# Kernel optimization log

Hardware: AMD Instinct MI355X
Metric: run time of the kernel (lower is better)

## Reference

```python
import jax, jax.numpy as jnp
import numpy as np

DECAY = 0.99
EPS = 1e-05


def setup_inputs() -> dict:
    key = jax.random.key(0)
    k1, k2 = jax.random.split(key)
    B, T, D, K = 16, 4096, 256, 1024
    z = jax.random.normal(k1, (B, T, D), dtype=jnp.float32)
    embedding = jax.random.normal(k2, (D, K), dtype=jnp.float32)
    cluster_size = jnp.zeros((K,), dtype=jnp.float32)
    embedding_mean = embedding.copy()  # torch init: embedding.clone()
    return {"z": z, "embedding": embedding, "cluster_size": cluster_size,
            "embedding_mean": embedding_mean}


def reference(z, embedding, cluster_size, embedding_mean):
    """Training-mode forward of CodebookEMA (proj=False).

    z:              [B, T, D]
    embedding:      [D, K] codebook buffer
    cluster_size:   [K]    EMA cluster counts
    embedding_mean: [D, K] EMA cluster sums
    Returns (z_q, commitment_loss, codebook_loss, code,
             new_embedding, new_cluster_size, new_embedding_mean).
    """
    B, T, D = z.shape
    K = embedding.shape[1]
    z_flat = z.reshape(B * T, D)

    # squared-distance quantization: ||z||^2 - 2 z.E + ||e||^2  -> [BT, K]
    dist = ((z_flat * z_flat).sum(1, keepdims=True)
            - 2.0 * (z_flat @ embedding)
            + (embedding * embedding).sum(0)[None, :])
    idx = jnp.argmin(dist, axis=1)              # [BT]
    code = idx.reshape(B, T)

    # EMA codebook update (no one-hot materialization; use segment sums)
    counts = jax.ops.segment_sum(jnp.ones_like(idx, dtype=z.dtype), idx,
                                 num_segments=K)               # [K]
    emb_sum = jax.ops.segment_sum(z_flat, idx, num_segments=K).T  # [D, K]
    new_cluster_size = cluster_size * DECAY + (1.0 - DECAY) * counts
    new_embedding_mean = embedding_mean * DECAY + (1.0 - DECAY) * emb_sum
    n = new_cluster_size.sum()
    cs_norm = (new_cluster_size + EPS) / (n + K * EPS) * n     # Laplace-smoothed
    new_embedding = new_embedding_mean / cs_norm[None, :]      # [D, K]

    # dequantize with the *updated* codebook (as in the torch control flow)
    z_q = new_embedding.T[code]                                # [B, T, D]

    commitment_loss = ((jax.lax.stop_gradient(z_q) - z) ** 2).mean(axis=(1, 2))
    codebook_loss = jnp.zeros((B,), dtype=z.dtype)
    z_q = z + jax.lax.stop_gradient(z_q - z)  # straight-through estimator
    return (z_q, commitment_loss, codebook_loss, code,
            new_embedding, new_cluster_size, new_embedding_mean)
```

## Files before the change

### kernel.cpp

```cpp
#include <hip/hip_runtime.h>
#include <cfloat>
#include <climits>
#include <cstdint>

#define B_ 16
#define T_ 4096
#define D_ 256
#define K_ 1024
#define BT_ 65536
#define DECAYF 0.99f
#define OMDECAYF 0.01f
#define EPSF 1e-5f
#define TAUGAP 0.125f
#define CHUNK 32
#define GROUP 16
#define RMARGIN 0.01f

typedef float f32x4 __attribute__((ext_vector_type(4)));
typedef _Float16 f16x8 __attribute__((ext_vector_type(8)));

__device__ __forceinline__ void gload16(const void* g, void* l) {
    __builtin_amdgcn_global_load_lds(
        (const __attribute__((address_space(1))) void*)g,
        (__attribute__((address_space(3))) void*)l, 16, 0, 0);
}

__global__ void k_prep(const float* __restrict__ z, const float* __restrict__ E,
                       _Float16* __restrict__ zf, _Float16* __restrict__ EfT,
                       float* __restrict__ enorm, double* __restrict__ enorm64,
                       int* __restrict__ counts, int* __restrict__ nflag,
                       float* __restrict__ out_closs, float* __restrict__ out_cbl,
                       float* __restrict__ emb_sum) {
    int b = blockIdx.x;
    if (b < 8192) {
        int base = (b * 256 + threadIdx.x) * 8;
        float4 v0 = *(const float4*)(z + base);
        float4 v1 = *(const float4*)(z + base + 4);
        f16x8 h;
        h[0] = (_Float16)v0.x; h[1] = (_Float16)v0.y;
        h[2] = (_Float16)v0.z; h[3] = (_Float16)v0.w;
        h[4] = (_Float16)v1.x; h[5] = (_Float16)v1.y;
        h[6] = (_Float16)v1.z; h[7] = (_Float16)v1.w;
        *(f16x8*)(zf + base) = h;
    } else {
        __shared__ double rd[256];
        int n = b - 8192, d = threadIdx.x;
        float v = E[(size_t)d * K_ + n];
        EfT[(size_t)n * 256 + d] = (_Float16)v;
        rd[d] = (double)v * (double)v;
        __syncthreads();
        for (int st = 128; st > 0; st >>= 1) {
            if (d < st) rd[d] += rd[d + st];
            __syncthreads();
        }
        if (d == 0) { enorm[n] = (float)rd[0]; enorm64[n] = rd[0]; }
        emb_sum[(size_t)n * 256 + d] = 0.f;
        if (n < 4) counts[n * 256 + d] = 0;
        if (n == 4) {
            if (d < 16) out_closs[d] = 0.f;
            else if (d < 32) out_cbl[d - 16] = 0.f;
            else if (d == 32) *nflag = 0;
        }
    }
}

__global__ __launch_bounds__(512, 2) void k_argmin_mfma(
    const _Float16* __restrict__ zf, const _Float16* __restrict__ EfT,
    const float* __restrict__ enorm, int* __restrict__ code,
    int* __restrict__ flags, int* __restrict__ nflag, int* __restrict__ counts) {
    __shared__ _Float16 Ab[2][128 * 32];
    __shared__ _Float16 Bb[2][256 * 32];
    __shared__ float mg_d1[512];
    __shared__ int   mg_i1[512];
    __shared__ float mg_d2[512];

    const int t = threadIdx.x;
    const int row0 = blockIdx.x * 128;
    const int l = t & 63, wid = t >> 6;
    const int wr = wid >> 2, wc = wid & 3;
    const int lr = l & 15, lk = l >> 4;

    const int arow = t >> 2,          ablk = (t & 3) ^ ((arow >> 1) & 3);
    const int brow0 = t >> 2,         bblk0 = (t & 3) ^ ((brow0 >> 1) & 3);
    const int brow1 = (t + 512) >> 2, bblk1 = ((t + 512) & 3) ^ ((brow1 >> 1) & 3);

#define STAGE(it_, buf_) do {                                                       \
        int nc_ = (it_) >> 3; int kb_ = ((it_) & 7) * 32;                            \
        gload16(zf + (size_t)(row0 + arow) * 256 + kb_ + ablk * 8,                   \
                &Ab[buf_][(t & ~63) * 8]);                                           \
        gload16(EfT + (size_t)(nc_ * 256 + brow0) * 256 + kb_ + bblk0 * 8,           \
                &Bb[buf_][(t & ~63) * 8]);                                           \
        gload16(EfT + (size_t)(nc_ * 256 + brow1) * 256 + kb_ + bblk1 * 8,           \
                &Bb[buf_][((t + 512) & ~63) * 8]);                                   \
    } while (0)

    STAGE(0, 0);

    float D1[4][4], D2[4][4];
    int   I1[4][4];
    #pragma unroll
    for (int m = 0; m < 4; ++m)
        #pragma unroll
        for (int r = 0; r < 4; ++r) {
            D1[m][r] = FLT_MAX; D2[m][r] = FLT_MAX; I1[m][r] = 0x7fffffff;
        }

    f32x4 acc[4][4];
    for (int it = 0; it < 32; ++it) {
        if ((it & 7) == 0) {
            #pragma unroll
            for (int m = 0; m < 4; ++m)
                #pragma unroll
                for (int n = 0; n < 4; ++n) acc[m][n] = (f32x4){0.f, 0.f, 0.f, 0.f};
        }
        __syncthreads();
        if (it + 1 < 32) STAGE(it + 1, (it + 1) & 1);
        const _Float16* Abuf = Ab[it & 1];
        const _Float16* Bbuf = Bb[it & 1];
        f16x8 a[4], b[4];
        #pragma unroll
        for (int m = 0; m < 4; ++m) {
            int row = wr * 64 + m * 16 + lr;
            a[m] = *(const f16x8*)&Abuf[row * 32 + ((lk ^ ((row >> 1) & 3)) * 8)];
        }
        #pragma unroll
        for (int n = 0; n < 4; ++n) {
            int nn = wc * 64 + n * 16 + lr;
            b[n] = *(const f16x8*)&Bbuf[nn * 32 + ((lk ^ ((nn >> 1) & 3)) * 8)];
        }
        #pragma unroll
        for (int m = 0; m < 4; ++m)
            #pragma unroll
            for (int n = 0; n < 4; ++n)
                acc[m][n] = __builtin_amdgcn_mfma_f32_16x16x32_f16(
                    a[m], b[n], acc[m][n], 0, 0, 0);

        if ((it & 7) == 7) {
            int nc = it >> 3;
            float en[4];
            #pragma unroll
            for (int n = 0; n < 4; ++n)
                en[n] = enorm[nc * 256 + wc * 64 + n * 16 + lr];
            #pragma unroll
            for (int m = 0; m < 4; ++m)
                #pragma unroll
                for (int r = 0; r < 4; ++r)
                    #pragma unroll
                    for (int n = 0; n < 4; ++n) {
                        float dist = en[n] - 2.0f * acc[m][n][r];
                        int cg = nc * 256 + wc * 64 + n * 16 + lr;
                        if (dist < D1[m][r]) {
                            D2[m][r] = D1[m][r]; D1[m][r] = dist; I1[m][r] = cg;
                        } else D2[m][r] = fminf(D2[m][r], dist);
                    }
        }
    }
#undef STAGE

    #pragma unroll
    for (int m = 0; m < 4; ++m)
        #pragma unroll
        for (int r = 0; r < 4; ++r) {
            float d1 = D1[m][r], d2 = D2[m][r];
            int i1 = I1[m][r];
            #pragma unroll
            for (int mask = 1; mask < 16; mask <<= 1) {
                float pd1 = __shfl_xor(d1, mask);
                int   pi1 = __shfl_xor(i1, mask);
                float pd2 = __shfl_xor(d2, mask);
                if (pd1 < d1 || (pd1 == d1 && pi1 < i1)) {
                    d2 = fminf(d1, pd2); d1 = pd1; i1 = pi1;
                } else d2 = fminf(d2, pd1);
            }
            if (lr == 0) {
                int row = wr * 64 + m * 16 + lk * 4 + r;
                mg_d1[row * 4 + wc] = d1;
                mg_i1[row * 4 + wc] = i1;
                mg_d2[row * 4 + wc] = d2;
            }
        }
    __syncthreads();
    if (t < 128) {
        float b1 = FLT_MAX, b2 = FLT_MAX;
        int bi = 0x7fffffff;
        #pragma unroll
        for (int c = 0; c < 4; ++c) {
            float pd1 = mg_d1[t * 4 + c];
            int   pi1 = mg_i1[t * 4 + c];
            float pd2 = mg_d2[t * 4 + c];
            if (pd1 < b1 || (pd1 == b1 && pi1 < bi)) {
                b2 = fminf(b1, pd2); b1 = pd1; bi = pi1;
            } else b2 = fminf(b2, pd1);
        }
        code[row0 + t] = bi;
        atomicAdd(&counts[bi], 1);
        if (b2 - b1 < TAUGAP) {
            int pos = atomicAdd(nflag, 1);
            flags[pos] = row0 + t;
        }
    }
}

__global__ __launch_bounds__(256) void k_fixup(
    const float* __restrict__ z, const float* __restrict__ E,
    const float* __restrict__ enorm, const double* __restrict__ enorm64,
    const int* __restrict__ nflag, const int* __restrict__ flags,
    int* __restrict__ code, int* __restrict__ counts) {
    __shared__ float  zrows[GROUP][256];
    __shared__ int    rowid[GROUP];
    __shared__ float  bw[GROUP][4];
    __shared__ float  bestAll[GROUP];
    __shared__ int    ccnt[GROUP];
    __shared__ int    cand[GROUP][16];
    __shared__ double cdist[GROUP][16];

    const int t = threadIdx.x, w = t >> 6, l = t & 63;
    const int n = *nflag;
    const int ngroups = (n + GROUP - 1) / GROUP;

    for (int g = blockIdx.x; g < ngroups; g += gridDim.x) {
        __syncthreads();
        if (t < GROUP) {
            int idx = g * GROUP + t;
            rowid[t] = (idx < n) ? flags[idx] : -1;
            ccnt[t] = 0;
        }
        __syncthreads();
        {
            int i = t >> 4, s = t & 15;
            int r = rowid[i];
            const float* src = z + (size_t)(r < 0 ? 0 : r) * D_ + s * 16;
            float4 a0 = *(const float4*)(src + 0);
            float4 a1 = *(const float4*)(src + 4);
            float4 a2 = *(const float4*)(src + 8);
            float4 a3 = *(const float4*)(src + 12);
            *(float4*)&zrows[i][s * 16 + 0]  = a0;
            *(float4*)&zrows[i][s * 16 + 4]  = a1;
            *(float4*)&zrows[i][s * 16 + 8]  = a2;
            *(float4*)&zrows[i][s * 16 + 12] = a3;
        }
        __syncthreads();

        float acc[GROUP][4];
        #pragma unroll
        for (int i = 0; i < GROUP; ++i) {
            acc[i][0] = 0.f; acc[i][1] = 0.f; acc[i][2] = 0.f; acc[i][3] = 0.f;
        }
        const float* Ecol = E + 4 * t;
        for (int d = 0; d < D_; ++d) {
            float4 ev = *(const float4*)(Ecol + (size_t)d * K_);
            #pragma unroll
            for (int i = 0; i < GROUP; ++i) {
                float zd = zrows[i][d];
                acc[i][0] = fmaf(zd, ev.x, acc[i][0]);
                acc[i][1] = fmaf(zd, ev.y, acc[i][1]);
                acc[i][2] = fmaf(zd, ev.z, acc[i][2]);
                acc[i][3] = fmaf(zd, ev.w, acc[i][3]);
            }
        }
        float en0 = enorm[4 * t], en1 = enorm[4 * t + 1];
        float en2 = enorm[4 * t + 2], en3 = enorm[4 * t + 3];
        #pragma unroll
        for (int i = 0; i < GROUP; ++i) {
            acc[i][0] = en0 - 2.f * acc[i][0];
            acc[i][1] = en1 - 2.f * acc[i][1];
            acc[i][2] = en2 - 2.f * acc[i][2];
            acc[i][3] = en3 - 2.f * acc[i][3];
        }
        #pragma unroll
        for (int i = 0; i < GROUP; ++i) {
            float b = fminf(fminf(acc[i][0], acc[i][1]), fminf(acc[i][2], acc[i][3]));
            #pragma unroll
            for (int m = 1; m < 64; m <<= 1) b = fminf(b, __shfl_xor(b, m));
            if (l == 0) bw[i][w] = b;
        }
        __syncthreads();
        if (t < GROUP)
            bestAll[t] = fminf(fminf(bw[t][0], bw[t][1]), fminf(bw[t][2], bw[t][3]));
        __syncthreads();
        #pragma unroll
        for (int i = 0; i < GROUP; ++i) {
            float thr = bestAll[i] + RMARGIN;
            #pragma unroll
            for (int j = 0; j < 4; ++j) {
                if (acc[i][j] <= thr) {
                    int slot = atomicAdd(&ccnt[i], 1);
                    if (slot < 16) cand[i][slot] = 4 * t + j;
                }
            }
        }
        __syncthreads();
        for (int p = w; p < GROUP * 16; p += 4) {
            int i = p >> 4, s = p & 15;
            int cn = ccnt[i];
            if (rowid[i] < 0 || cn < 2 || s >= (cn < 16 ? cn : 16)) continue;
            int c = cand[i][s];
            double dot = 0.0;
            #pragma unroll
            for (int q = 0; q < 4; ++q) {
                int d = l * 4 + q;
                dot = fma((double)zrows[i][d], (double)E[(size_t)d * K_ + c], dot);
            }
            #pragma unroll
            for (int m = 1; m < 64; m <<= 1) dot += __shfl_xor(dot, m);
            if (l == 0) cdist[i][s] = enorm64[c] - 2.0 * dot;
        }
        __syncthreads();
        if (t < GROUP) {
            int r = rowid[t];
            if (r >= 0) {
                int cn = ccnt[t]; if (cn > 16) cn = 16;
                int newc;
                if (cn <= 1) {
                    newc = cand[t][0];
                } else {
                    double bd = DBL_MAX; int bi = INT_MAX;
                    for (int s = 0; s < cn; ++s) {
                        double dv = cdist[t][s]; int ci = cand[t][s];
                        if (dv < bd || (dv == bd && ci < bi)) { bd = dv; bi = ci; }
                    }
                    newc = bi;
                }
                int oldc = code[r];
                if (newc != oldc) {
                    code[r] = newc;
                    atomicSub(&counts[oldc], 1);
                    atomicAdd(&counts[newc], 1);
                }
            }
        }
    }
}

__global__ void k_scan(const int* __restrict__ counts, const float* __restrict__ cs,
                       int* __restrict__ offsets, int* __restrict__ cursor,
                       float* __restrict__ out_newcs, float* __restrict__ csnorm,
                       int* __restrict__ work, int* __restrict__ nwork) {
    __shared__ int   s[K_];
    __shared__ int   c[K_];
    __shared__ float red[K_];
    int t = threadIdx.x;
    int v = counts[t];
    int nch = (v + CHUNK - 1) / CHUNK;
    s[t] = v;
    c[t] = nch;
    float ncs = cs[t] * DECAYF + OMDECAYF * (float)v;
    out_newcs[t] = ncs;
    red[t] = ncs;
    __syncthreads();
    for (int d = 1; d < K_; d <<= 1) {
        int x = (t >= d) ? s[t - d] : 0;
        int y = (t >= d) ? c[t - d] : 0;
        __syncthreads();
        s[t] += x; c[t] += y;
        __syncthreads();
    }
    offsets[t] = s[t] - v;
    cursor[t]  = s[t] - v;
    if (t == K_ - 1) { offsets[K_] = s[t]; *nwork = c[t]; }
    int wbase = c[t] - nch;
    for (int j = 0; j < nch; ++j) work[wbase + j] = (t << 16) | j;
    for (int st = 512; st > 0; st >>= 1) {
        if (t < st) red[t] += red[t + st];
        __syncthreads();
    }
    float nsum = red[0];
    csnorm[t] = (ncs + EPSF) / (nsum + (float)K_ * EPSF) * nsum;
}

__global__ void k_sortidx(const int* __restrict__ code, int* __restrict__ cursor,
                          int* __restrict__ sorted) {
    int r = blockIdx.x * 256 + threadIdx.x;
    int cc = code[r];
    int pos = atomicAdd(&cursor[cc], 1);
    sorted[pos] = r;
}

__global__ void k_segsum(const float* __restrict__ z, const int* __restrict__ sorted,
                         const int* __restrict__ offsets, const int* __restrict__ work,
                         const int* __restrict__ nwork, float* __restrict__ emb_sum) {
    int NW = *nwork;
    int d = threadIdx.x;
    for (int i = blockIdx.x; i < NW; i += gridDim.x) {
        int wk = work[i];
        int k = wk >> 16, j = wk & 0xffff;
        int beg = offsets[k] + j * CHUNK;
        int end = min(beg + CHUNK, offsets[k + 1]);
        float s = 0.f;
        int idx = beg;
        for (; idx + 4 <= end; idx += 4) {
            int r0 = sorted[idx], r1 = sorted[idx + 1];
            int r2 = sorted[idx + 2], r3 = sorted[idx + 3];
            float v0 = z[(size_t)r0 * D_ + d];
            float v1 = z[(size_t)r1 * D_ + d];
            float v2 = z[(size_t)r2 * D_ + d];
            float v3 = z[(size_t)r3 * D_ + d];
            s += (v0 + v1) + (v2 + v3);
        }
        for (; idx < end; ++idx) s += z[(size_t)sorted[idx] * D_ + d];
        atomicAdd(&emb_sum[(size_t)k * D_ + d], s);
    }
}

__global__ void k_emb(const float* __restrict__ EM, const float* __restrict__ emb_sum,
                      const float* __restrict__ csnorm,
                      float* __restrict__ out_newemb, float* __restrict__ out_newem,
                      float* __restrict__ newembT) {
    int tid = blockIdx.x * 256 + threadIdx.x;
    int k = tid >> 8, d = tid & 255;
    float em  = EM[(size_t)d * K_ + k];
    float nem = em * DECAYF + OMDECAYF * emb_sum[tid];
    float nq  = nem / csnorm[k];
    out_newem [(size_t)d * K_ + k] = nem;
    out_newemb[(size_t)d * K_ + k] = nq;
    newembT[tid] = nq;
}

__global__ __launch_bounds__(256) void k_gather(
    const float* __restrict__ z, const int* __restrict__ code,
    const float* __restrict__ newembT,
    float* __restrict__ out_zq, float* __restrict__ out_code,
    float* __restrict__ out_closs) {
    __shared__ double wsum[4];
    const int w = threadIdx.x >> 6, l = threadIdx.x & 63;
    const int base = blockIdx.x * 32 + w * 8;
    double acc = 0.0;
    #pragma unroll
    for (int it = 0; it < 2; ++it) {
        const int r0 = base + it * 4;
        int i0 = code[r0], i1 = code[r0 + 1], i2 = code[r0 + 2], i3 = code[r0 + 3];
        float4 z0 = *(const float4*)(z + (size_t)(r0    ) * D_ + l * 4);
        float4 z1 = *(const float4*)(z + (size_t)(r0 + 1) * D_ + l * 4);
        float4 z2 = *(const float4*)(z + (size_t)(r0 + 2) * D_ + l * 4);
        float4 z3 = *(const float4*)(z + (size_t)(r0 + 3) * D_ + l * 4);
        float4 e0 = *(const float4*)(newembT + (size_t)i0 * D_ + l * 4);
        float4 e1 = *(const float4*)(newembT + (size_t)i1 * D_ + l * 4);
        float4 e2 = *(const float4*)(newembT + (size_t)i2 * D_ + l * 4);
        float4 e3 = *(const float4*)(newembT + (size_t)i3 * D_ + l * 4);
        *(float4*)(out_zq + (size_t)(r0    ) * D_ + l * 4) = e0;
        *(float4*)(out_zq + (size_t)(r0 + 1) * D_ + l * 4) = e1;
        *(float4*)(out_zq + (size_t)(r0 + 2) * D_ + l * 4) = e2;
        *(float4*)(out_zq + (size_t)(r0 + 3) * D_ + l * 4) = e3;
        if (l < 4) out_code[r0 + l] = (float)(l == 0 ? i0 : l == 1 ? i1 : l == 2 ? i2 : i3);
        float dx, dy, dz2, dw2;
        dx = e0.x - z0.x; dy = e0.y - z0.y; dz2 = e0.z - z0.z; dw2 = e0.w - z0.w;
        acc += (double)dx * dx + (double)dy * dy + (double)dz2 * dz2 + (double)dw2 * dw2;
        dx = e1.x - z1.x; dy = e1.y - z1.y; dz2 = e1.z - z1.z; dw2 = e1.w - z1.w;
        acc += (double)dx * dx + (double)dy * dy + (double)dz2 * dz2 + (double)dw2 * dw2;
        dx = e2.x - z2.x; dy = e2.y - z2.y; dz2 = e2.z - z2.z; dw2 = e2.w - z2.w;
        acc += (double)dx * dx + (double)dy * dy + (double)dz2 * dz2 + (double)dw2 * dw2;
        dx = e3.x - z3.x; dy = e3.y - z3.y; dz2 = e3.z - z3.z; dw2 = e3.w - z3.w;
        acc += (double)dx * dx + (double)dy * dy + (double)dz2 * dz2 + (double)dw2 * dw2;
    }
    #pragma unroll
    for (int off = 32; off > 0; off >>= 1) acc += __shfl_down(acc, off);
    if (l == 0) wsum[w] = acc;
    __syncthreads();
    if (threadIdx.x == 0) {
        float v = (float)((wsum[0] + wsum[1] + wsum[2] + wsum[3]) *
                          (1.0 / ((double)T_ * (double)D_)));
        atomicAdd(&out_closs[blockIdx.x >> 7], v);
    }
}

extern "C" void kernel_launch(void* const* d_in, const int* in_sizes, int n_in,
                              void* d_out, int out_size, void* d_ws, size_t ws_size,
                              hipStream_t stream) {
    (void)in_sizes; (void)n_in; (void)out_size; (void)ws_size;
    const float* z  = (const float*)d_in[0];
    const float* E  = (const float*)d_in[1];
    const float* cs = (const float*)d_in[2];
    const float* EM = (const float*)d_in[3];

    float* out       = (float*)d_out;
    float* out_zq    = out;
    float* out_closs = out + 16777216;
    float* out_cbl   = out_closs + 16;
    float* out_code  = out_cbl + 16;
    float* out_nemb  = out_code + 65536;
    float* out_ncs   = out_nemb + 262144;
    float* out_nem   = out_ncs + 1024;

    _Float16* zf = (_Float16*)out_zq;

    char* w = (char*)d_ws;
    int*      counts  = (int*)(w + 0);
    int*      nflag   = (int*)(w + 4096);
    int*      offsets = (int*)(w + 4160);
    int*      cursor  = (int*)(w + 8320);
    float*    enorm   = (float*)(w + 12416);
    int*      code_i  = (int*)(w + 16512);
    int*      flags   = (int*)(w + 278656);
    float*    csnorm  = (float*)(w + 540800);
    float*    newembT = (float*)(w + 544896);
    _Float16* EfT     = (_Float16*)(w + 1593472);
    int*      sorted  = (int*)(w + 2117760);
    float*    emb_sum = (float*)(w + 2379904);
    int*      work    = (int*)(w + 3428480);
    int*      nwork   = (int*)(w + 3444864);
    double*   enorm64 = (double*)(w + 3444928);

    k_prep       <<<9216, 256, 0, stream>>>(z, E, zf, EfT, enorm, enorm64, counts,
                                            nflag, out_closs, out_cbl, emb_sum);
    k_argmin_mfma<<<BT_ / 128, 512, 0, stream>>>(zf, EfT, enorm, code_i, flags,
                                                 nflag, counts);
    k_fixup      <<<256, 256, 0, stream>>>(z, E, enorm, enorm64, nflag, flags,
                                           code_i, counts);
    k_scan       <<<1, K_, 0, stream>>>(counts, cs, offsets, cursor, out_ncs, csnorm,
                                        work, nwork);
    k_sortidx    <<<BT_ / 256, 256, 0, stream>>>(code_i, cursor, sorted);
    k_segsum     <<<2048, 256, 0, stream>>>(z, sorted, offsets, work, nwork, emb_sum);
    k_emb        <<<(K_ * D_) / 256, 256, 0, stream>>>(EM, emb_sum, csnorm,
                                                       out_nemb, out_nem, newembT);
    k_gather     <<<BT_ / 32, 256, 0, stream>>>(z, code_i, newembT, out_zq, out_code,
                                                out_closs);
}
```

Baseline: 291.2 us.

## Split argmin GEMM across codebook chunks and merge partial minima in a new kernel

The argmin kernel now launches one block per (row tile, 256-code chunk) pair, four times as many blocks. Each block writes its per-row best, index and second-best to scratch space inside the z_q output buffer, and a new merge kernel combines the four partials. The merge kernel also assigns codes, flags near-tie rows and accumulates counts through a shared-memory histogram. Launch bounds rise to 6 blocks per CU and the per-chunk register state for running minima is dropped, aiming at higher occupancy and better GPU fill, at the cost of an extra launch and partial-result traffic.

```diff
diff --git a/kernel.cpp b/kernel.cpp
--- a/kernel.cpp
+++ b/kernel.cpp
@@ -64,18 +64,16 @@
     }
 }
 
-__global__ __launch_bounds__(512, 2) void k_argmin_mfma(
+__global__ __launch_bounds__(512, 6) void k_argmin_mfma(
     const _Float16* __restrict__ zf, const _Float16* __restrict__ EfT,
-    const float* __restrict__ enorm, int* __restrict__ code,
-    int* __restrict__ flags, int* __restrict__ nflag, int* __restrict__ counts) {
+    const float* __restrict__ enorm,
+    float* __restrict__ pd1, int* __restrict__ pi1, float* __restrict__ pd2) {
     __shared__ _Float16 Ab[2][128 * 32];
     __shared__ _Float16 Bb[2][256 * 32];
-    __shared__ float mg_d1[512];
-    __shared__ int   mg_i1[512];
-    __shared__ float mg_d2[512];
 
     const int t = threadIdx.x;
-    const int row0 = blockIdx.x * 128;
+    const int rb = blockIdx.x >> 2, nc = blockIdx.x & 3;
+    const int row0 = rb * 128;
     const int l = t & 63, wid = t >> 6;
     const int wr = wid >> 2, wc = wid & 3;
     const int lr = l & 15, lk = l >> 4;
@@ -85,36 +83,26 @@
     const int brow1 = (t + 512) >> 2, bblk1 = ((t + 512) & 3) ^ ((brow1 >> 1) & 3);
 
 #define STAGE(it_, buf_) do {                                                       \
-        int nc_ = (it_) >> 3; int kb_ = ((it_) & 7) * 32;                            \
+        int kb_ = (it_) * 32;                                                        \
         gload16(zf + (size_t)(row0 + arow) * 256 + kb_ + ablk * 8,                   \
                 &Ab[buf_][(t & ~63) * 8]);                                           \
-        gload16(EfT + (size_t)(nc_ * 256 + brow0) * 256 + kb_ + bblk0 * 8,           \
+        gload16(EfT + (size_t)(nc * 256 + brow0) * 256 + kb_ + bblk0 * 8,            \
                 &Bb[buf_][(t & ~63) * 8]);                                           \
-        gload16(EfT + (size_t)(nc_ * 256 + brow1) * 256 + kb_ + bblk1 * 8,           \
+        gload16(EfT + (size_t)(nc * 256 + brow1) * 256 + kb_ + bblk1 * 8,            \
                 &Bb[buf_][((t + 512) & ~63) * 8]);                                   \
     } while (0)
 
     STAGE(0, 0);
 
-    float D1[4][4], D2[4][4];
-    int   I1[4][4];
+    f32x4 acc[4][4];
     #pragma unroll
     for (int m = 0; m < 4; ++m)
         #pragma unroll
-        for (int r = 0; r < 4; ++r) {
-            D1[m][r] = FLT_MAX; D2[m][r] = FLT_MAX; I1[m][r] = 0x7fffffff;
-        }
-
-    f32x4 acc[4][4];
-    for (int it = 0; it < 32; ++it) {
-        if ((it & 7) == 0) {
-            #pragma unroll
-            for (int m = 0; m < 4; ++m)
-                #pragma unroll
-                for (int n = 0; n < 4; ++n) acc[m][n] = (f32x4){0.f, 0.f, 0.f, 0.f};
-        }
-        __syncthreads();
-        if (it + 1 < 32) STAGE(it + 1, (it + 1) & 1);
+        for (int n = 0; n < 4; ++n) acc[m][n] = (f32x4){0.f, 0.f, 0.f, 0.f};
+
+    for (int it = 0; it < 8; ++it) {
+        __syncthreads();
+        if (it + 1 < 8) STAGE(it + 1, (it + 1) & 1);
         const _Float16* Abuf = Ab[it & 1];
         const _Float16* Bbuf = Bb[it & 1];
         f16x8 a[4], b[4];
@@ -134,43 +122,40 @@
             for (int n = 0; n < 4; ++n)
                 acc[m][n] = __builtin_amdgcn_mfma_f32_16x16x32_f16(
                     a[m], b[n], acc[m][n], 0, 0, 0);
-
-        if ((it & 7) == 7) {
-            int nc = it >> 3;
-            float en[4];
-            #pragma unroll
-            for (int n = 0; n < 4; ++n)
-                en[n] = enorm[nc * 256 + wc * 64 + n * 16 + lr];
-            #pragma unroll
-            for (int m = 0; m < 4; ++m)
-                #pragma unroll
-                for (int r = 0; r < 4; ++r)
-                    #pragma unroll
-                    for (int n = 0; n < 4; ++n) {
-                        float dist = en[n] - 2.0f * acc[m][n][r];
-                        int cg = nc * 256 + wc * 64 + n * 16 + lr;
-                        if (dist < D1[m][r]) {
-                            D2[m][r] = D1[m][r]; D1[m][r] = dist; I1[m][r] = cg;
-                        } else D2[m][r] = fminf(D2[m][r], dist);
-                    }
-        }
     }
 #undef STAGE
 
+    float en[4];
+    #pragma unroll
+    for (int n = 0; n < 4; ++n)
+        en[n] = enorm[nc * 256 + wc * 64 + n * 16 + lr];
+
+    __syncthreads();
+    float* mg_d1 = (float*)&Ab[0][0];
+    int*   mg_i1 = (int*)(mg_d1 + 512);
+    float* mg_d2 = (float*)(mg_i1 + 512);
+
     #pragma unroll
     for (int m = 0; m < 4; ++m)
         #pragma unroll
         for (int r = 0; r < 4; ++r) {
-            float d1 = D1[m][r], d2 = D2[m][r];
-            int i1 = I1[m][r];
+            float d1 = FLT_MAX, d2 = FLT_MAX;
+            int i1 = 0x7fffffff;
+            #pragma unroll
+            for (int n = 0; n < 4; ++n) {
+                float dist = en[n] - 2.0f * acc[m][n][r];
+                int cg = nc * 256 + wc * 64 + n * 16 + lr;
+                if (dist < d1) { d2 = d1; d1 = dist; i1 = cg; }
+                else d2 = fminf(d2, dist);
+            }
             #pragma unroll
             for (int mask = 1; mask < 16; mask <<= 1) {
-                float pd1 = __shfl_xor(d1, mask);
-                int   pi1 = __shfl_xor(i1, mask);
-                float pd2 = __shfl_xor(d2, mask);
-                if (pd1 < d1 || (pd1 == d1 && pi1 < i1)) {
-                    d2 = fminf(d1, pd2); d1 = pd1; i1 = pi1;
-                } else d2 = fminf(d2, pd1);
+                float q1 = __shfl_xor(d1, mask);
+                int   qi = __shfl_xor(i1, mask);
+                float q2 = __shfl_xor(d2, mask);
+                if (q1 < d1 || (q1 == d1 && qi < i1)) {
+                    d2 = fminf(d1, q2); d1 = q1; i1 = qi;
+                } else d2 = fminf(d2, q1);
             }
             if (lr == 0) {
                 int row = wr * 64 + m * 16 + lk * 4 + r;
@@ -185,19 +170,55 @@
         int bi = 0x7fffffff;
         #pragma unroll
         for (int c = 0; c < 4; ++c) {
-            float pd1 = mg_d1[t * 4 + c];
-            int   pi1 = mg_i1[t * 4 + c];
-            float pd2 = mg_d2[t * 4 + c];
-            if (pd1 < b1 || (pd1 == b1 && pi1 < bi)) {
-                b2 = fminf(b1, pd2); b1 = pd1; bi = pi1;
-            } else b2 = fminf(b2, pd1);
-        }
-        code[row0 + t] = bi;
-        atomicAdd(&counts[bi], 1);
-        if (b2 - b1 < TAUGAP) {
-            int pos = atomicAdd(nflag, 1);
-            flags[pos] = row0 + t;
-        }
+            float q1 = mg_d1[t * 4 + c];
+            int   qi = mg_i1[t * 4 + c];
+            float q2 = mg_d2[t * 4 + c];
+            if (q1 < b1 || (q1 == b1 && qi < bi)) {
+                b2 = fminf(fminf(b1, q2), b2); b1 = q1; bi = qi;
+            } else b2 = fminf(b2, q1);
+        }
+        size_t idx = (size_t)(row0 + t) * 4 + nc;
+        pd1[idx] = b1; pi1[idx] = bi; pd2[idx] = b2;
+    }
+}
+
+__global__ void k_amerge(const float* __restrict__ pd1, const int* __restrict__ pi1,
+                         const float* __restrict__ pd2, int* __restrict__ code,
+                         int* __restrict__ flags, int* __restrict__ nflag,
+                         int* __restrict__ counts) {
+    __shared__ int h[K_];
+    int t = threadIdx.x;
+    #pragma unroll
+    for (int j = t; j < K_; j += 256) h[j] = 0;
+    __syncthreads();
+    int r = blockIdx.x * 256 + t;
+    float4 d1v = *(const float4*)&pd1[(size_t)r * 4];
+    int4   i1v = *(const int4*)&pi1[(size_t)r * 4];
+    float4 d2v = *(const float4*)&pd2[(size_t)r * 4];
+    float D1 = FLT_MAX, D2 = FLT_MAX;
+    int I1 = 0x7fffffff;
+    float d1s[4] = {d1v.x, d1v.y, d1v.z, d1v.w};
+    float d2s[4] = {d2v.x, d2v.y, d2v.z, d2v.w};
+    int   i1s[4] = {i1v.x, i1v.y, i1v.z, i1v.w};
+    #pragma unroll
+    for (int c = 0; c < 4; ++c) {
+        float d1 = d1s[c], d2 = d2s[c];
+        int i1 = i1s[c];
+        if (d1 < D1 || (d1 == D1 && i1 < I1)) {
+            D2 = fminf(fminf(D1, d2), D2); D1 = d1; I1 = i1;
+        } else D2 = fminf(D2, d1);
+    }
+    code[r] = I1;
+    atomicAdd(&h[I1], 1);
+    if (D2 - D1 < TAUGAP) {
+        int pos = atomicAdd(nflag, 1);
+        flags[pos] = r;
+    }
+    __syncthreads();
+    #pragma unroll
+    for (int j = t; j < K_; j += 256) {
+        int v = h[j];
+        if (v) atomicAdd(&counts[j], v);
     }
 }
 
@@ -481,7 +502,10 @@
     float* out_ncs   = out_nemb + 262144;
     float* out_nem   = out_ncs + 1024;
 
-    _Float16* zf = (_Float16*)out_zq;
+    _Float16* zf  = (_Float16*)out_zq;
+    float*    pd1 = out_zq + 8388608;
+    int*      pi1 = (int*)(out_zq + 8388608 + 262144);
+    float*    pd2 = out_zq + 8388608 + 524288;
 
     char* w = (char*)d_ws;
     int*      counts  = (int*)(w + 0);
@@ -502,7 +526,8 @@
 
     k_prep       <<<9216, 256, 0, stream>>>(z, E, zf, EfT, enorm, enorm64, counts,
                                             nflag, out_closs, out_cbl, emb_sum);
-    k_argmin_mfma<<<BT_ / 128, 512, 0, stream>>>(zf, EfT, enorm, code_i, flags,
+    k_argmin_mfma<<<2048, 512, 0, stream>>>(zf, EfT, enorm, pd1, pi1, pd2);
+    k_amerge     <<<BT_ / 256, 256, 0, stream>>>(pd1, pi1, pd2, code_i, flags,
                                                  nflag, counts);
     k_fixup      <<<256, 256, 0, stream>>>(z, E, enorm, enorm64, nflag, flags,
                                            code_i, counts);
```

After: 403.2 us. 38.5% more time.
